# Performance work log

Measured on AMD Instinct MI355X. Metric: run time of the kernel, lower is better.

## Reference

```python
import jax, jax.numpy as jnp
import numpy as np

D_MODEL = 1024
NUM_HEADS = 16
HEAD_DIM = D_MODEL // NUM_HEADS
SEQ_LEN = 2048
THETA = 10000.0


def setup_inputs() -> dict:
    key = jax.random.key(0)
    ks = jax.random.split(key, 9)
    s = 1.0 / np.sqrt(D_MODEL)
    inp = {
        "x": jax.random.normal(ks[0], (2, SEQ_LEN, D_MODEL), dtype=jnp.float32),
        "Wq": jax.random.uniform(ks[1], (D_MODEL, D_MODEL), jnp.float32, -s, s),
        "bq": jax.random.uniform(ks[2], (D_MODEL,), jnp.float32, -s, s),
        "Wk": jax.random.uniform(ks[3], (D_MODEL, D_MODEL), jnp.float32, -s, s),
        "bk": jax.random.uniform(ks[4], (D_MODEL,), jnp.float32, -s, s),
        "Wv": jax.random.uniform(ks[5], (D_MODEL, D_MODEL), jnp.float32, -s, s),
        "bv": jax.random.uniform(ks[6], (D_MODEL,), jnp.float32, -s, s),
        "Wo": jax.random.uniform(ks[7], (D_MODEL, D_MODEL), jnp.float32, -s, s),
        "bo": jax.random.uniform(ks[8], (D_MODEL,), jnp.float32, -s, s),
    }
    return inp


def _rope_cos_sin(seq_len, dim, theta):
    inv_freq = 1.0 / theta ** (jnp.arange(0, dim, 2, dtype=jnp.float32) / dim)  # [dim/2]
    t = jnp.arange(seq_len, dtype=jnp.float32)
    freqs = jnp.outer(t, inv_freq)  # [S, dim/2]
    return jnp.cos(freqs), jnp.sin(freqs)


def _apply_rope(x, cos, sin):
    # x: [B, H, S, head_dim]; interleaved complex pairs (even, odd)
    x2 = x.reshape(*x.shape[:-1], -1, 2)  # [B,H,S,hd/2,2]
    xe, xo = x2[..., 0], x2[..., 1]
    c = cos[None, None, :, :]
    s = sin[None, None, :, :]
    oe = xe * c - xo * s
    oo = xe * s + xo * c
    return jnp.stack([oe, oo], axis=-1).reshape(x.shape)


def reference(x, Wq, bq, Wk, bk, Wv, bv, Wo, bo):
    B, S, D = x.shape
    H, hd = NUM_HEADS, HEAD_DIM
    q = x @ Wq.T + bq
    k = x @ Wk.T + bk
    v = x @ Wv.T + bv
    # [B, H, S, hd]
    q = q.reshape(B, S, H, hd).transpose(0, 2, 1, 3)
    k = k.reshape(B, S, H, hd).transpose(0, 2, 1, 3)
    v = v.reshape(B, S, H, hd).transpose(0, 2, 1, 3)
    cos, sin = _rope_cos_sin(S, hd, THETA)
    q = _apply_rope(q, cos, sin)
    k = _apply_rope(k, cos, sin)
    scores = jnp.einsum("bhqd,bhkd->bhqk", q, k) / jnp.sqrt(jnp.float32(hd))
    causal = jnp.triu(jnp.ones((S, S), dtype=bool), k=1)
    scores = jnp.where(causal[None, None, :, :], -jnp.inf, scores)
    attn = jax.nn.softmax(scores, axis=-1)
    out = jnp.einsum("bhqk,bhkd->bhqd", attn, v)
    out = out.transpose(0, 2, 1, 3).reshape(B, S, D)
    return out @ Wo.T + bo
```

## Files before the change

### kernel.cpp

```cpp
#include <hip/hip_runtime.h>
#include <hip/hip_bf16.h>

#define S_LEN 2048
#define DM 1024
#define NH 16
#define HD 64
#define M_ROWS 4096
#define LOG2E 1.4426950408889634f
#define MASKVAL -1.0e4f
#define QSCALE 0.18033688011112042f

typedef __attribute__((ext_vector_type(8))) short short8;
typedef __attribute__((ext_vector_type(2))) float f32x2;
typedef __attribute__((ext_vector_type(4))) float f32x4;
typedef __attribute__((ext_vector_type(16))) float f32x16;

__device__ inline ushort f2b(float f) {
  union { float f; unsigned u; } v; v.f = f;
  unsigned r = v.u + 0x7fffu + ((v.u >> 16) & 1u);
  return (ushort)(r >> 16);
}

__device__ inline float b2f(ushort u) {
  union { unsigned u; float f; } v; v.u = ((unsigned)u) << 16; return v.f;
}

__device__ inline unsigned pk_bf16(float a, float b) {
  __hip_bfloat162 h = __float22bfloat162_rn(make_float2(a, b));
  union { __hip_bfloat162 h; unsigned u; } v; v.h = h;
  return v.u;
}

__device__ inline float fexp2(float x) { return __builtin_amdgcn_exp2f(x); }

__device__ inline void gl_lds16(const void* g, void* l) {
  __builtin_amdgcn_global_load_lds(
      (const __attribute__((address_space(1))) void*)g,
      (__attribute__((address_space(3))) void*)l, 16, 0, 0);
}

__global__ __launch_bounds__(256) void cast_rope_kernel(
    const float* __restrict__ x, const float* __restrict__ Wq, const float* __restrict__ Wk,
    const float* __restrict__ Wv, const float* __restrict__ Wo,
    ushort* __restrict__ xb, ushort* __restrict__ Wqb, ushort* __restrict__ Wkb,
    ushort* __restrict__ Wvb, ushort* __restrict__ Wob,
    float* __restrict__ ropeC, float* __restrict__ ropeS) {
  const int bid = blockIdx.x;
  if (bid >= 8192) {
    int idx = (bid - 8192) * 256 + threadIdx.x;
    int s = idx >> 5, i = idx & 31;
    float inv = exp2f(-(float)i * (13.287712379549449f / 32.0f));
    float a = (float)s * inv;
    ropeC[idx] = cosf(a);
    ropeS[idx] = sinf(a);
    return;
  }
  int i = bid * 256 + threadIdx.x;
  int r = i >> 18, off = i & 0x3FFFF;
  const float4* s;
  uint2* d;
  switch (r) {
    case 0: case 1: case 2: case 3: s = (const float4*)x + i;  d = (uint2*)xb + i;  break;
    case 4: s = (const float4*)Wq + off; d = (uint2*)Wqb + off; break;
    case 5: s = (const float4*)Wk + off; d = (uint2*)Wkb + off; break;
    case 6: s = (const float4*)Wv + off; d = (uint2*)Wvb + off; break;
    default: s = (const float4*)Wo + off; d = (uint2*)Wob + off; break;
  }
  float4 v = *s;
  uint2 o;
  o.x = pk_bf16(v.x, v.y);
  o.y = pk_bf16(v.z, v.w);
  *d = o;
}

__global__ __launch_bounds__(256) void gemm_qkv_kernel(const ushort* __restrict__ xb,
    const ushort* __restrict__ Wqb, const ushort* __restrict__ Wkb, const ushort* __restrict__ Wvb,
    const float* __restrict__ bq, const float* __restrict__ bk, const float* __restrict__ bv,
    const float* __restrict__ ropeC, const float* __restrict__ ropeS,
    ushort* __restrict__ qb, ushort* __restrict__ kb, ushort* __restrict__ vT) {
  __shared__ ushort lds[32768];
  const int lid = blockIdx.x;
  const int xcd = lid & 7;
  const int idx = lid >> 3;
  const int z = idx >> 5;
  const int rem = idx & 31;
  const int mi = ((xcd & 3) << 3) | (rem & 7);
  const int ni = ((xcd >> 2) << 2) | (rem >> 3);
  const int m0 = mi * 128, n0 = ni * 128;
  const ushort* W = (z == 0) ? Wqb : ((z == 1) ? Wkb : Wvb);
  const float* bias = (z == 0) ? bq : ((z == 1) ? bk : bv);
  const int t = threadIdx.x, lane = t & 63, wave = t >> 6;
  const int wr = (wave >> 1) * 64, wc = (wave & 1) * 64;
  const int lr = lane & 15, lg = lane >> 4;

  const int slot0 = wave * 128 + lane, slot1 = slot0 + 64;
  const int row0 = slot0 >> 2, g0 = (slot0 & 3) ^ (row0 & 3);
  const int row1 = slot1 >> 2, g1 = (slot1 & 3) ^ (row1 & 3);
  const ushort* Ap0 = &xb[(size_t)(m0 + row0) * DM + g0 * 8];
  const ushort* Ap1 = &xb[(size_t)(m0 + row1) * DM + g1 * 8];
  const ushort* Wp0 = &W[(size_t)(n0 + row0) * DM + g0 * 8];
  const ushort* Wp1 = &W[(size_t)(n0 + row1) * DM + g1 * 8];

  f32x4 acc[4][4];
#pragma unroll
  for (int a = 0; a < 4; a++)
#pragma unroll
    for (int b = 0; b < 4; b++) acc[a][b] = (f32x4){0.f, 0.f, 0.f, 0.f};

#pragma unroll
  for (int ha = 0; ha < 2; ++ha) {
    const int k0 = ha * 32;
    gl_lds16(Ap0 + k0, &lds[ha * 4096 + slot0 * 8]);
    gl_lds16(Ap1 + k0, &lds[ha * 4096 + slot1 * 8]);
    gl_lds16(Wp0 + k0, &lds[16384 + ha * 4096 + slot0 * 8]);
    gl_lds16(Wp1 + k0, &lds[16384 + ha * 4096 + slot1 * 8]);
  }
  asm volatile("s_waitcnt vmcnt(0)" ::: "memory");
  __builtin_amdgcn_s_barrier();
  __builtin_amdgcn_sched_barrier(0);

  int buf = 0;
  for (int j = 0; j < 16; ++j) {
    const bool pref = (j + 1 < 16);
    if (pref) {
      const int nb = (buf ^ 1) * 8192;
#pragma unroll
      for (int ha = 0; ha < 2; ++ha) {
        const int k0 = (2 * j + 2 + ha) * 32;
        gl_lds16(Ap0 + k0, &lds[nb + ha * 4096 + slot0 * 8]);
        gl_lds16(Ap1 + k0, &lds[nb + ha * 4096 + slot1 * 8]);
        gl_lds16(Wp0 + k0, &lds[16384 + nb + ha * 4096 + slot0 * 8]);
        gl_lds16(Wp1 + k0, &lds[16384 + nb + ha * 4096 + slot1 * 8]);
      }
    }
#pragma unroll
    for (int ha = 0; ha < 2; ++ha) {
      const int fb = buf * 8192 + ha * 4096;
      short8 af[4], bf[4];
#pragma unroll
      for (int mt = 0; mt < 4; mt++) {
        const int row = wr + mt * 16 + lr;
        af[mt] = *(const short8*)&lds[fb + (row * 4 + (lg ^ (row & 3))) * 8];
      }
#pragma unroll
      for (int nt = 0; nt < 4; nt++) {
        const int row = wc + nt * 16 + lr;
        bf[nt] = *(const short8*)&lds[16384 + fb + (row * 4 + (lg ^ (row & 3))) * 8];
      }
#pragma unroll
      for (int mt = 0; mt < 4; mt++)
#pragma unroll
        for (int nt = 0; nt < 4; nt++)
          acc[mt][nt] = __builtin_amdgcn_mfma_f32_16x16x32_bf16(af[mt], bf[nt], acc[mt][nt], 0, 0, 0);
    }
    if (pref) {
      asm volatile("s_waitcnt vmcnt(0)" ::: "memory");
      __builtin_amdgcn_s_barrier();
      __builtin_amdgcn_sched_barrier(0);
    }
    buf ^= 1;
  }
  __syncthreads();

#pragma unroll
  for (int mt = 0; mt < 4; mt++) {
#pragma unroll
    for (int nt = 0; nt < 4; nt++) {
      const int nloc = wc + nt * 16 + lr;
      const float bn = bias[n0 + nloc];
#pragma unroll
      for (int r = 0; r < 4; r++) {
        const int mloc = wr + mt * 16 + lg * 4 + r;
        const ushort v = f2b(acc[mt][nt][r] + bn);
        if (z < 2) lds[mloc * 136 + nloc] = v;
        else       lds[nloc * 136 + mloc] = v;
      }
    }
  }
  __syncthreads();

  const int b = m0 >> 11;
  if (z < 2) {
    ushort* dst = (z == 0) ? qb : kb;
    const float qscale = (z == 0) ? QSCALE : 1.0f;
#pragma unroll
    for (int c = 0; c < 8; c++) {
      const int sloc = c * 16 + (t >> 4);
      const int nloc = (t & 15) * 8;
      short8 val = *(const short8*)&lds[sloc * 136 + nloc];
      const int s = (m0 + sloc) & (S_LEN - 1);
      const int h = (n0 + nloc) >> 6;
      const int d0 = nloc & 63;
      const float4 cv = *(const float4*)&ropeC[s * 32 + d0 / 2];
      const float4 sv = *(const float4*)&ropeS[s * 32 + d0 / 2];
      uint4 o;
      {
        float e = b2f((ushort)val[0]), od = b2f((ushort)val[1]);
        o.x = pk_bf16((e * cv.x - od * sv.x) * qscale, (e * sv.x + od * cv.x) * qscale);
      }
      {
        float e = b2f((ushort)val[2]), od = b2f((ushort)val[3]);
        o.y = pk_bf16((e * cv.y - od * sv.y) * qscale, (e * sv.y + od * cv.y) * qscale);
      }
      {
        float e = b2f((ushort)val[4]), od = b2f((ushort)val[5]);
        o.z = pk_bf16((e * cv.z - od * sv.z) * qscale, (e * sv.z + od * cv.z) * qscale);
      }
      {
        float e = b2f((ushort)val[6]), od = b2f((ushort)val[7]);
        o.w = pk_bf16((e * cv.w - od * sv.w) * qscale, (e * sv.w + od * cv.w) * qscale);
      }
      *(uint4*)&dst[(((size_t)b * NH + h) * S_LEN + s) * HD + d0] = o;
    }
  } else {
    const int sbase = m0 & (S_LEN - 1);
#pragma unroll
    for (int c = 0; c < 8; c++) {
      const int nloc = c * 16 + (t >> 4);
      const int s0 = (t & 15) * 8;
      short8 val = *(const short8*)&lds[nloc * 136 + s0];
      const int h = (n0 + nloc) >> 6;
      const int d = nloc & 63;
      *(short8*)&vT[(((size_t)b * NH + h) * HD + d) * S_LEN + sbase + s0] = val;
    }
  }
}

__global__ __launch_bounds__(256) void flash_kernel(const ushort* __restrict__ qb,
                                                    const ushort* __restrict__ kb,
                                                    const ushort* __restrict__ vT,
                                                    ushort* __restrict__ attn) {
  __shared__ ushort lds[32768];
  const int t = threadIdx.x, lane = t & 63, wave = t >> 6;
  const int q31 = lane & 31, h = lane >> 5;
  const int lid = blockIdx.x;
  const int g = lid >> 5;
  const int qt = (g < 8) ? (15 - g) : (g - 8);
  const int bh = lid & 31;
  const int q0 = qt * 128;
  const int nint = qt + 1;

  const ushort* kbh = kb + (size_t)bh * S_LEN * HD;
  const ushort* vbh = vT + (size_t)bh * HD * S_LEN;

  const int qrow = q0 + wave * 32 + q31;
  const ushort* qptr = qb + ((size_t)bh * S_LEN + qrow) * HD + h * 8;
  short8 qf[4];
#pragma unroll
  for (int s = 0; s < 4; s++) qf[s] = *(const short8*)(qptr + s * 16);

  const int slot0 = wave * 128 + lane, slot1 = slot0 + 64;
  const int row0 = slot0 >> 3, g0 = (slot0 & 7) ^ (row0 & 7);
  const int row1 = slot1 >> 3, g1 = (slot1 & 7) ^ (row1 & 7);
  const int lo0 = wave * 128 * 8, lo1 = lo0 + 64 * 8;

  int foff[4][2];
#pragma unroll
  for (int s = 0; s < 4; s++)
#pragma unroll
    for (int st = 0; st < 2; st++) {
      const int row = st * 32 + q31;
      foff[s][st] = (row * 8 + ((2 * s + h) ^ (row & 7))) * 8;
    }

  const ushort* kp0 = kbh + (size_t)row0 * HD + g0 * 8;
  const ushort* kp1 = kbh + (size_t)row1 * HD + g1 * 8;
  const ushort* vp0 = vbh + (size_t)row0 * S_LEN + g0 * 8;
  const ushort* vp1 = vbh + (size_t)row1 * S_LEN + g1 * 8;

#pragma unroll
  for (int ha = 0; ha < 2; ++ha) {
    gl_lds16(kp0, &lds[ha * 4096 + lo0]);
    gl_lds16(kp1, &lds[ha * 4096 + lo1]);
    gl_lds16(vp0, &lds[16384 + ha * 4096 + lo0]);
    gl_lds16(vp1, &lds[16384 + ha * 4096 + lo1]);
    kp0 += 64 * HD; kp1 += 64 * HD; vp0 += 64; vp1 += 64;
  }

  f32x16 O[2];
#pragma unroll
  for (int st = 0; st < 2; st++)
#pragma unroll
    for (int r = 0; r < 16; r++) O[st][r] = 0.f;

  f32x16 zc;
#pragma unroll
  for (int r = 0; r < 16; r++) zc[r] = 0.f;

  f32x2 lpA = (f32x2){0.f, 0.f}, lpB = (f32x2){0.f, 0.f};

  asm volatile("s_waitcnt vmcnt(0)" ::: "memory");
  __builtin_amdgcn_s_barrier();
  __builtin_amdgcn_sched_barrier(0);

  int buf = 0;
  for (int j = 0; j < nint; ++j) {
    const bool pref = (j + 1 < nint);
    if (pref) {
      const int nb = (buf ^ 1) * 8192;
#pragma unroll
      for (int ha = 0; ha < 2; ++ha) {
        gl_lds16(kp0, &lds[nb + ha * 4096 + lo0]);
        gl_lds16(kp1, &lds[nb + ha * 4096 + lo1]);
        gl_lds16(vp0, &lds[16384 + nb + ha * 4096 + lo0]);
        gl_lds16(vp1, &lds[16384 + nb + ha * 4096 + lo1]);
        kp0 += 64 * HD; kp1 += 64 * HD; vp0 += 64; vp1 += 64;
      }
    }

#pragma unroll
    for (int ha = 0; ha < 2; ++ha) {
      const ushort* Kb = &lds[buf * 8192 + ha * 4096];
      const ushort* Vb = &lds[16384 + buf * 8192 + ha * 4096];
      const int kt = 2 * j + ha;

      f32x16 sc0, sc1;
      __builtin_amdgcn_s_setprio(1);
      sc0 = __builtin_amdgcn_mfma_f32_32x32x16_bf16(
          *(const short8*)&Kb[foff[0][0]], qf[0], zc, 0, 0, 0);
      sc1 = __builtin_amdgcn_mfma_f32_32x32x16_bf16(
          *(const short8*)&Kb[foff[0][1]], qf[0], zc, 0, 0, 0);
#pragma unroll
      for (int s = 1; s < 4; s++) {
        sc0 = __builtin_amdgcn_mfma_f32_32x32x16_bf16(
            *(const short8*)&Kb[foff[s][0]], qf[s], sc0, 0, 0, 0);
        sc1 = __builtin_amdgcn_mfma_f32_32x32x16_bf16(
            *(const short8*)&Kb[foff[s][1]], qf[s], sc1, 0, 0, 0);
      }
      __builtin_amdgcn_s_setprio(0);

      if (kt * 64 + 63 > q0 + wave * 32) {
#pragma unroll
        for (int r = 0; r < 16; r++) {
          const int kc0 = kt * 64 + (r & 3) + 8 * (r >> 2) + 4 * h;
          if (kc0 > qrow) sc0[r] = MASKVAL;
          if (kc0 + 32 > qrow) sc1[r] = MASKVAL;
        }
      }
#pragma unroll
      for (int r = 0; r < 16; r += 2) {
        const float a0 = fexp2(sc0[r]), a1 = fexp2(sc0[r + 1]);
        const float b0 = fexp2(sc1[r]), b1 = fexp2(sc1[r + 1]);
        sc0[r] = a0; sc0[r + 1] = a1;
        sc1[r] = b0; sc1[r + 1] = b1;
        lpA += (f32x2){a0, a1};
        lpB += (f32x2){b0, b1};
      }

      unsigned pp[8][2];
#pragma unroll
      for (int rg = 0; rg < 4; rg++) {
        pp[rg][0] = pk_bf16(sc0[4 * rg + 0], sc0[4 * rg + 1]);
        pp[rg][1] = pk_bf16(sc0[4 * rg + 2], sc0[4 * rg + 3]);
        pp[4 + rg][0] = pk_bf16(sc1[4 * rg + 0], sc1[4 * rg + 1]);
        pp[4 + rg][1] = pk_bf16(sc1[4 * rg + 2], sc1[4 * rg + 3]);
      }
      __builtin_amdgcn_s_setprio(1);
#pragma unroll
      for (int s = 0; s < 4; s++) {
        unsigned d0 = pp[2 * s][0], e0 = pp[2 * s + 1][0];
        unsigned d1 = pp[2 * s][1], e1 = pp[2 * s + 1][1];
        asm("v_permlane32_swap_b32 %0, %1" : "+v"(d0), "+v"(e0));
        asm("v_permlane32_swap_b32 %0, %1" : "+v"(d1), "+v"(e1));
        union { unsigned u[4]; short8 v; } pf;
        pf.u[0] = d0;
        pf.u[1] = d1;
        pf.u[2] = e0;
        pf.u[3] = e1;
        O[0] = __builtin_amdgcn_mfma_f32_32x32x16_bf16(
            *(const short8*)&Vb[foff[s][0]], pf.v, O[0], 0, 0, 0);
        O[1] = __builtin_amdgcn_mfma_f32_32x32x16_bf16(
            *(const short8*)&Vb[foff[s][1]], pf.v, O[1], 0, 0, 0);
      }
      __builtin_amdgcn_s_setprio(0);
    }

    if (pref) {
      asm volatile("s_waitcnt vmcnt(0)" ::: "memory");
      __builtin_amdgcn_s_barrier();
      __builtin_amdgcn_sched_barrier(0);
    }
    buf ^= 1;
  }

  float lacc = (lpA[0] + lpA[1]) + (lpB[0] + lpB[1]);
  lacc += __shfl_xor(lacc, 32);
  const float inv = 1.f / lacc;

  const int b = bh >> 4, hh = bh & 15;
  const int q = q0 + wave * 32 + q31;
  ushort* obase = attn + ((size_t)b * S_LEN + q) * DM + hh * HD;
#pragma unroll
  for (int st = 0; st < 2; st++)
#pragma unroll
    for (int rg = 0; rg < 4; rg++) {
      const int d0 = st * 32 + 8 * rg + 4 * h;
      uint2 w;
      w.x = pk_bf16(O[st][4 * rg + 0] * inv, O[st][4 * rg + 1] * inv);
      w.y = pk_bf16(O[st][4 * rg + 2] * inv, O[st][4 * rg + 3] * inv);
      *(uint2*)&obase[d0] = w;
    }
}

__global__ __launch_bounds__(256) void gemm_out_kernel(const ushort* __restrict__ attn,
                                                       const ushort* __restrict__ Wob,
                                                       const float* __restrict__ bo,
                                                       float* __restrict__ out) {
  __shared__ ushort lds[24576];
  const int lid = blockIdx.x;
  const int xcd = lid & 7;
  const int idx = lid >> 3;
  const int mi = ((xcd & 3) << 3) | (idx & 7);
  const int ni = ((xcd >> 2) << 3) | (idx >> 3);
  const int m0 = mi * 128, n0 = ni * 64;
  const int t = threadIdx.x, lane = t & 63, wave = t >> 6;
  const int wm = (wave >> 1) * 64, wn = (wave & 1) * 32;
  const int lr = lane & 15, lg = lane >> 4;
  const int slotA0 = wave * 128 + lane, slotA1 = slotA0 + 64;
  const int rowA0 = slotA0 >> 2, gA0 = (slotA0 & 3) ^ (rowA0 & 3);
  const int rowA1 = slotA1 >> 2, gA1 = (slotA1 & 3) ^ (rowA1 & 3);
  const int slotB = wave * 64 + lane;
  const int rowB = slotB >> 2, gB = (slotB & 3) ^ (rowB & 3);
  const ushort* Ap0 = &attn[(size_t)(m0 + rowA0) * DM + gA0 * 8];
  const ushort* Ap1 = &attn[(size_t)(m0 + rowA1) * DM + gA1 * 8];
  const ushort* Wp  = &Wob[(size_t)(n0 + rowB) * DM + gB * 8];

  f32x4 acc[4][2];
#pragma unroll
  for (int a = 0; a < 4; a++)
#pragma unroll
    for (int b = 0; b < 2; b++) acc[a][b] = (f32x4){0.f, 0.f, 0.f, 0.f};

#pragma unroll
  for (int ha = 0; ha < 2; ++ha) {
    const int k0 = ha * 32;
    gl_lds16(Ap0 + k0, &lds[ha * 4096 + slotA0 * 8]);
    gl_lds16(Ap1 + k0, &lds[ha * 4096 + slotA1 * 8]);
    gl_lds16(Wp + k0, &lds[16384 + ha * 2048 + slotB * 8]);
  }
  asm volatile("s_waitcnt vmcnt(0)" ::: "memory");
  __builtin_amdgcn_s_barrier();
  __builtin_amdgcn_sched_barrier(0);

  int buf = 0;
  for (int j = 0; j < 16; ++j) {
    const bool pref = (j + 1 < 16);
    if (pref) {
      const int nbA = (buf ^ 1) * 8192;
      const int nbB = 16384 + (buf ^ 1) * 4096;
#pragma unroll
      for (int ha = 0; ha < 2; ++ha) {
        const int k0 = (2 * j + 2 + ha) * 32;
        gl_lds16(Ap0 + k0, &lds[nbA + ha * 4096 + slotA0 * 8]);
        gl_lds16(Ap1 + k0, &lds[nbA + ha * 4096 + slotA1 * 8]);
        gl_lds16(Wp + k0, &lds[nbB + ha * 2048 + slotB * 8]);
      }
    }
#pragma unroll
    for (int ha = 0; ha < 2; ++ha) {
      const int fbA = buf * 8192 + ha * 4096;
      const int fbB = 16384 + buf * 4096 + ha * 2048;
      short8 af[4], bf[2];
#pragma unroll
      for (int mt = 0; mt < 4; mt++) {
        const int row = wm + mt * 16 + lr;
        af[mt] = *(const short8*)&lds[fbA + (row * 4 + (lg ^ (row & 3))) * 8];
      }
#pragma unroll
      for (int nt = 0; nt < 2; nt++) {
        const int row = wn + nt * 16 + lr;
        bf[nt] = *(const short8*)&lds[fbB + (row * 4 + (lg ^ (row & 3))) * 8];
      }
#pragma unroll
      for (int mt = 0; mt < 4; mt++)
#pragma unroll
        for (int nt = 0; nt < 2; nt++)
          acc[mt][nt] = __builtin_amdgcn_mfma_f32_16x16x32_bf16(af[mt], bf[nt], acc[mt][nt], 0, 0, 0);
    }
    if (pref) {
      asm volatile("s_waitcnt vmcnt(0)" ::: "memory");
      __builtin_amdgcn_s_barrier();
      __builtin_amdgcn_sched_barrier(0);
    }
    buf ^= 1;
  }

#pragma unroll
  for (int mt = 0; mt < 4; mt++) {
#pragma unroll
    for (int nt = 0; nt < 2; nt++) {
      const int n = n0 + wn + nt * 16 + lr;
      const float bn = bo[n];
#pragma unroll
      for (int r = 0; r < 4; r++) {
        const int m = m0 + wm + mt * 16 + lg * 4 + r;
        out[(size_t)m * DM + n] = acc[mt][nt][r] + bn;
      }
    }
  }
}

extern "C" void kernel_launch(void* const* d_in, const int* in_sizes, int n_in,
                              void* d_out, int out_size, void* d_ws, size_t ws_size,
                              hipStream_t stream) {
  const float* x  = (const float*)d_in[0];
  const float* Wq = (const float*)d_in[1];
  const float* bq = (const float*)d_in[2];
  const float* Wk = (const float*)d_in[3];
  const float* bk = (const float*)d_in[4];
  const float* Wv = (const float*)d_in[5];
  const float* bv = (const float*)d_in[6];
  const float* Wo = (const float*)d_in[7];
  const float* bo = (const float*)d_in[8];
  float* out = (float*)d_out;

  char* ws = (char*)d_ws;
  size_t off = 0;
  auto alloc = [&](size_t bytes) { char* p = ws + off; off += (bytes + 255) & ~255ull; return p; };
  ushort* xb   = (ushort*)alloc((size_t)M_ROWS * DM * 2);
  ushort* Wqb  = (ushort*)alloc((size_t)DM * DM * 2);
  ushort* Wkb  = (ushort*)alloc((size_t)DM * DM * 2);
  ushort* Wvb  = (ushort*)alloc((size_t)DM * DM * 2);
  ushort* Wob  = (ushort*)alloc((size_t)DM * DM * 2);
  ushort* qb   = (ushort*)alloc((size_t)M_ROWS * DM * 2);
  ushort* kb   = (ushort*)alloc((size_t)M_ROWS * DM * 2);
  ushort* vTb  = (ushort*)alloc((size_t)M_ROWS * DM * 2);
  ushort* attn = (ushort*)alloc((size_t)M_ROWS * DM * 2);
  float* ropeC = (float*)alloc((size_t)S_LEN * 32 * 4);
  float* ropeS = (float*)alloc((size_t)S_LEN * 32 * 4);
  (void)ws_size; (void)in_sizes; (void)n_in; (void)out_size;

  cast_rope_kernel<<<8448, 256, 0, stream>>>(x, Wq, Wk, Wv, Wo, xb, Wqb, Wkb, Wvb, Wob,
                                             ropeC, ropeS);
  gemm_qkv_kernel<<<768, 256, 0, stream>>>(
      xb, Wqb, Wkb, Wvb, bq, bk, bv, ropeC, ropeS, qb, kb, vTb);
  flash_kernel<<<512, 256, 0, stream>>>(qb, kb, vTb, attn);
  gemm_out_kernel<<<512, 256, 0, stream>>>(attn, Wob, bo, out);
}
```

Measured before the change: 184.4 us.

## Use triple-buffered LDS ring with two-stage prefetch in output projection GEMM

The output-projection GEMM moves from double buffering over 64-wide K chunks to a 3-slot ring of 32-wide K chunks, prefetching two stages ahead. It waits with vmcnt(3) so one load group can stay in flight across each barrier, which should hide more global-load latency. LDS use drops from 48KB to 36KB, which may allow more resident blocks. The cost is twice as many barriers per K sweep and less MFMA work between syncs.

```diff
diff --git a/kernel.cpp b/kernel.cpp
--- a/kernel.cpp
+++ b/kernel.cpp
@@ -406,7 +406,7 @@
                                                        const ushort* __restrict__ Wob,
                                                        const float* __restrict__ bo,
                                                        float* __restrict__ out) {
-  __shared__ ushort lds[24576];
+  __shared__ ushort lds[18432];
   const int lid = blockIdx.x;
   const int xcd = lid & 7;
   const int idx = lid >> 3;
@@ -431,58 +431,49 @@
 #pragma unroll
     for (int b = 0; b < 2; b++) acc[a][b] = (f32x4){0.f, 0.f, 0.f, 0.f};
 
-#pragma unroll
-  for (int ha = 0; ha < 2; ++ha) {
-    const int k0 = ha * 32;
-    gl_lds16(Ap0 + k0, &lds[ha * 4096 + slotA0 * 8]);
-    gl_lds16(Ap1 + k0, &lds[ha * 4096 + slotA1 * 8]);
-    gl_lds16(Wp + k0, &lds[16384 + ha * 2048 + slotB * 8]);
-  }
-  asm volatile("s_waitcnt vmcnt(0)" ::: "memory");
+  gl_lds16(Ap0, &lds[slotA0 * 8]);
+  gl_lds16(Ap1, &lds[slotA1 * 8]);
+  gl_lds16(Wp, &lds[12288 + slotB * 8]);
+  gl_lds16(Ap0 + 32, &lds[4096 + slotA0 * 8]);
+  gl_lds16(Ap1 + 32, &lds[4096 + slotA1 * 8]);
+  gl_lds16(Wp + 32, &lds[14336 + slotB * 8]);
+  asm volatile("s_waitcnt vmcnt(3)" ::: "memory");
   __builtin_amdgcn_s_barrier();
   __builtin_amdgcn_sched_barrier(0);
 
-  int buf = 0;
-  for (int j = 0; j < 16; ++j) {
-    const bool pref = (j + 1 < 16);
+  int cur = 0;
+  for (int i = 0; i < 32; i++) {
+    const bool pref = (i + 2 < 32);
     if (pref) {
-      const int nbA = (buf ^ 1) * 8192;
-      const int nbB = 16384 + (buf ^ 1) * 4096;
-#pragma unroll
-      for (int ha = 0; ha < 2; ++ha) {
-        const int k0 = (2 * j + 2 + ha) * 32;
-        gl_lds16(Ap0 + k0, &lds[nbA + ha * 4096 + slotA0 * 8]);
-        gl_lds16(Ap1 + k0, &lds[nbA + ha * 4096 + slotA1 * 8]);
-        gl_lds16(Wp + k0, &lds[nbB + ha * 2048 + slotB * 8]);
-      }
-    }
-#pragma unroll
-    for (int ha = 0; ha < 2; ++ha) {
-      const int fbA = buf * 8192 + ha * 4096;
-      const int fbB = 16384 + buf * 4096 + ha * 2048;
-      short8 af[4], bf[2];
-#pragma unroll
-      for (int mt = 0; mt < 4; mt++) {
-        const int row = wm + mt * 16 + lr;
-        af[mt] = *(const short8*)&lds[fbA + (row * 4 + (lg ^ (row & 3))) * 8];
-      }
-#pragma unroll
-      for (int nt = 0; nt < 2; nt++) {
-        const int row = wn + nt * 16 + lr;
-        bf[nt] = *(const short8*)&lds[fbB + (row * 4 + (lg ^ (row & 3))) * 8];
-      }
-#pragma unroll
-      for (int mt = 0; mt < 4; mt++)
-#pragma unroll
-        for (int nt = 0; nt < 2; nt++)
-          acc[mt][nt] = __builtin_amdgcn_mfma_f32_16x16x32_bf16(af[mt], bf[nt], acc[mt][nt], 0, 0, 0);
-    }
-    if (pref) {
-      asm volatile("s_waitcnt vmcnt(0)" ::: "memory");
+      const int nb = (cur >= 1) ? cur - 1 : 2;
+      const int k0 = (i + 2) * 32;
+      gl_lds16(Ap0 + k0, &lds[nb * 4096 + slotA0 * 8]);
+      gl_lds16(Ap1 + k0, &lds[nb * 4096 + slotA1 * 8]);
+      gl_lds16(Wp + k0, &lds[12288 + nb * 2048 + slotB * 8]);
+    }
+    short8 af[4], bf[2];
+#pragma unroll
+    for (int mt = 0; mt < 4; mt++) {
+      const int row = wm + mt * 16 + lr;
+      af[mt] = *(const short8*)&lds[cur * 4096 + (row * 4 + (lg ^ (row & 3))) * 8];
+    }
+#pragma unroll
+    for (int nt = 0; nt < 2; nt++) {
+      const int row = wn + nt * 16 + lr;
+      bf[nt] = *(const short8*)&lds[12288 + cur * 2048 + (row * 4 + (lg ^ (row & 3))) * 8];
+    }
+#pragma unroll
+    for (int mt = 0; mt < 4; mt++)
+#pragma unroll
+      for (int nt = 0; nt < 2; nt++)
+        acc[mt][nt] = __builtin_amdgcn_mfma_f32_16x16x32_bf16(af[mt], bf[nt], acc[mt][nt], 0, 0, 0);
+    if (i + 1 < 32) {
+      if (pref) asm volatile("s_waitcnt vmcnt(3)" ::: "memory");
+      else      asm volatile("s_waitcnt vmcnt(0)" ::: "memory");
       __builtin_amdgcn_s_barrier();
       __builtin_amdgcn_sched_barrier(0);
     }
-    buf ^= 1;
+    cur = (cur >= 2) ? 0 : cur + 1;
   }
 
 #pragma unroll
```

New measurement: 182.1 us. No clear change (-1.2%).
